# Kernel optimization log

Hardware: AMD Instinct MI355X
Metric: run time of the kernel (lower is better)

## Reference

```python
import jax, jax.numpy as jnp
import numpy as np

N, E, NG, H, BD, L, B = 4000, 50000, 12, 128, 128, 2, 100

def _gelu(x):
    return jax.nn.gelu(x, approximate=False)

def forward(pos, vel, charges, grid0, rand_SO3, batch, edge_index,
            W_basis1, b_basis1, W_basis2, b_basis2,
            W_fbasis1, b_fbasis1, W_fbasis2, b_fbasis2,
            W_embed, W_conv, W_fiber, b_conv, ln_gamma, ln_beta,
            W_ff1, b_ff1, W_ff2, b_ff2, W_ro1, b_ro1, W_ro2, b_ro2):
    n_nodes = pos.shape[0]
    n_graphs = rand_SO3.shape[0]
    n = grid0.shape[0]
    src, dst = edge_index[0], edge_index[1]
    # per-graph randomly rotated S2 grid
    grid_graph = jnp.einsum('bij,nj->bni', rand_SO3, grid0)    # [B,n,3]
    grid_node = grid_graph[batch]                               # [N,n,3]
    grid_edge = grid_node[src]                                  # [E,n,3]
    # R3S2 Euclidean invariants (separable): parallel + perpendicular parts of rel_pos wrt each grid orientation
    rel = pos[src] - pos[dst]                                   # [E,3]
    inv1 = jnp.einsum('ed,end->en', rel, grid_edge)[..., None]  # [E,n,1]
    inv2 = jnp.linalg.norm(rel[:, None, :] - inv1 * grid_edge, axis=-1, keepdims=True)
    cp = (charges[src] * charges[dst])[:, None, :]              # [E,1,1]
    ei = jnp.concatenate([inv1, inv2, jnp.broadcast_to(cp, inv1.shape)], -1)  # [E,n,3]
    # PolynomialFeatures(degree=2): [x, flatten(x outer x)] -> 3+9=12
    ei_poly = jnp.concatenate([ei, (ei[..., :, None] * ei[..., None, :]).reshape(ei.shape[:-1] + (9,))], -1)
    basis = _gelu(_gelu(ei_poly @ W_basis1 + b_basis1) @ W_basis2 + b_basis2)  # [E,n,BD]
    # fiber invariants: pairwise grid dot products (rotation cancels) -> [n,n,1]; poly deg 2 -> [n,n,2]
    fi = jnp.sum(grid0[:, None, :] * grid0[None, :, :], -1, keepdims=True)
    fi_poly = jnp.concatenate([fi, fi * fi], -1)
    fiber_basis = _gelu(_gelu(fi_poly @ W_fbasis1 + b_fbasis1) @ W_fbasis2 + b_fbasis2)  # [n,n,BD]
    # node features projected to sphere
    ones = jnp.ones((n_nodes, 1), pos.dtype)
    cnt = jax.ops.segment_sum(ones, batch, num_segments=n_graphs)
    mean_pos = jax.ops.segment_sum(pos, batch, num_segments=n_graphs) / jnp.maximum(cnt, 1.0)
    rel_pos = pos - mean_pos[batch]
    v_sph = jnp.einsum('nd,nkd->nk', vel, grid_node)[..., None]
    p_sph = jnp.einsum('nd,nkd->nk', rel_pos, grid_node)[..., None]
    c_sph = jnp.broadcast_to(charges[:, None, :], (n_nodes, n, 1))
    vn = jnp.linalg.norm(vel, axis=-1, keepdims=True)
    vn_sph = jnp.broadcast_to(vn[:, None, :], (n_nodes, n, 1))
    x = jnp.concatenate([v_sph, p_sph, c_sph, vn_sph], -1) @ W_embed  # [N,n,H]
    # SeparableBundleConvNext stack
    for l in range(W_conv.shape[0]):
        kern = basis @ W_conv[l]                                       # [E,n,H]
        x1 = jax.ops.segment_sum(x[src] * kern, dst, num_segments=n_nodes)  # depthwise spatial conv + scatter-add
        fk = fiber_basis @ W_fiber[l]                                  # [n,n,H]
        x2 = jnp.einsum('boc,poc->bpc', x1, fk) / n + b_conv[l]        # depthwise fiber conv
        mu = jnp.mean(x2, -1, keepdims=True)
        var = jnp.mean((x2 - mu) ** 2, -1, keepdims=True)
        h = (x2 - mu) / jnp.sqrt(var + 1e-5) * ln_gamma[l] + ln_beta[l]
        h = _gelu(h @ W_ff1[l] + b_ff1[l]) @ W_ff2[l] + b_ff2[l]
        x = x + h
    y = _gelu(x @ W_ro1 + b_ro1) @ W_ro2 + b_ro2                       # [N,n,1]
    return jnp.mean(grid_node * y, axis=-2)                            # sphere2vec -> [N,3]

def setup_inputs():
    key = jax.random.key(0)
    ks = jax.random.split(key, 24)
    f = jnp.float32
    # deterministic uniform-ish S2 grid (fibonacci sphere)
    i = np.arange(NG) + 0.5
    phi = np.arccos(1.0 - 2.0 * i / NG)
    th = np.pi * (1.0 + 5.0 ** 0.5) * i
    grid0 = jnp.asarray(np.stack([np.sin(phi) * np.cos(th), np.sin(phi) * np.sin(th), np.cos(phi)], -1), f)
    # random SO(3) per graph via unit quaternions
    q = jax.random.normal(ks[0], (B, 4), f)
    q = q / jnp.linalg.norm(q, axis=-1, keepdims=True)
    w, xq, yq, zq = q[:, 0], q[:, 1], q[:, 2], q[:, 3]
    R = jnp.stack([
        jnp.stack([1 - 2 * (yq ** 2 + zq ** 2), 2 * (xq * yq - zq * w), 2 * (xq * zq + yq * w)], -1),
        jnp.stack([2 * (xq * yq + zq * w), 1 - 2 * (xq ** 2 + zq ** 2), 2 * (yq * zq - xq * w)], -1),
        jnp.stack([2 * (xq * zq - yq * w), 2 * (yq * zq + xq * w), 1 - 2 * (xq ** 2 + yq ** 2)], -1)], -2)
    s = 0.05
    return dict(
        pos=jax.random.normal(ks[1], (N, 3), f),
        vel=jax.random.normal(ks[2], (N, 3), f),
        charges=jax.random.normal(ks[3], (N, 1), f),
        batch=jnp.sort(jax.random.randint(ks[4], (N,), 0, B)),
        edge_index=jax.random.randint(ks[5], (2, E), 0, N),
        grid0=grid0, rand_SO3=R,
        W_basis1=jax.random.normal(ks[6], (12, H), f) * s, b_basis1=jnp.zeros((H,), f),
        W_basis2=jax.random.normal(ks[7], (H, BD), f) * s, b_basis2=jnp.zeros((BD,), f),
        W_fbasis1=jax.random.normal(ks[8], (2, H), f) * s, b_fbasis1=jnp.zeros((H,), f),
        W_fbasis2=jax.random.normal(ks[9], (H, BD), f) * s, b_fbasis2=jnp.zeros((BD,), f),
        W_embed=jax.random.normal(ks[10], (4, H), f) * s,
        W_conv=jax.random.normal(ks[11], (L, BD, H), f) * s,
        W_fiber=jax.random.normal(ks[12], (L, BD, H), f) * s,
        b_conv=jnp.zeros((L, H), f),
        ln_gamma=jnp.ones((L, H), f), ln_beta=jnp.zeros((L, H), f),
        W_ff1=jax.random.normal(ks[13], (L, H, 4 * H), f) * s, b_ff1=jnp.zeros((L, 4 * H), f),
        W_ff2=jax.random.normal(ks[14], (L, 4 * H, H), f) * s, b_ff2=jnp.zeros((L, H), f),
        W_ro1=jax.random.normal(ks[15], (H, H), f) * s, b_ro1=jnp.zeros((H,), f),
        W_ro2=jax.random.normal(ks[16], (H, 1), f) * s, b_ro2=jnp.zeros((1,), f),
    )

def reference(pos, vel, charges, batch, edge_index, grid0, rand_SO3,
              W_basis1, b_basis1, W_basis2, b_basis2,
              W_fbasis1, b_fbasis1, W_fbasis2, b_fbasis2,
              W_embed, W_conv, W_fiber, b_conv, ln_gamma, ln_beta,
              W_ff1, b_ff1, W_ff2, b_ff2, W_ro1, b_ro1, W_ro2, b_ro2):
    return forward(pos, vel, charges, grid0, rand_SO3, batch, edge_index,
                   W_basis1, b_basis1, W_basis2, b_basis2,
                   W_fbasis1, b_fbasis1, W_fbasis2, b_fbasis2,
                   W_embed, W_conv, W_fiber, b_conv, ln_gamma, ln_beta,
                   W_ff1, b_ff1, W_ff2, b_ff2, W_ro1, b_ro1, W_ro2, b_ro2)
```

## Files before the change

kernel.cpp:

```cpp
#include <hip/hip_runtime.h>

typedef unsigned short u16;
typedef short s16x8 __attribute__((ext_vector_type(8)));
typedef float f32x4 __attribute__((ext_vector_type(4)));

constexpr int NNODES = 4000;
constexpr int NEDGES = 50000;
constexpr int NGRID  = 12;
constexpr int HD     = 128;
constexpr int H4     = 512;
constexpr int NLAY   = 2;

constexpr size_t OFF_GN   = 0;
constexpr size_t OFF_PS   = 144000;
constexpr size_t OFF_CNT  = 144304;
constexpr size_t OFF_FK   = 144512;
constexpr size_t OFF_X    = 181376;
constexpr size_t OFF_X1   = 6325376;
constexpr size_t OFF_WB   = 12469376;
constexpr size_t OFF_ROWP = 12625024;
constexpr size_t OFF_DEG  = 12629032;
constexpr size_t OFF_CUR  = 12633032;
constexpr size_t OFF_ESRT = 12637032;
constexpr size_t OFF_EIPB = 12687032;
constexpr size_t OFF_W1T  = 17487416;
constexpr size_t OFF_SRCS = 17489464;
constexpr size_t OFF_END_SLOW = 17539464;
constexpr size_t OFF_BAS  = 17539464;
constexpr size_t KERN_F   = 38400000;
constexpr size_t OFF_END_FAST  = OFF_BAS + KERN_F;
constexpr size_t OFF_END_DUAL  = OFF_BAS + 2*KERN_F;

constexpr size_t WB_W2T = 0;
constexpr size_t WB_WCT = 16384;
constexpr size_t WB_F1T = 49152;
constexpr size_t WB_F2T = 180224;

__device__ __forceinline__ u16 f2bf(float f){
  union { float f; unsigned int i; } v; v.f = f;
  unsigned int x = v.i;
  x += 0x7fffu + ((x >> 16) & 1u);
  return (u16)(x >> 16);
}
__device__ __forceinline__ float bf2f(u16 u){
  union { unsigned int i; float f; } v; v.i = ((unsigned int)u) << 16; return v.f;
}
__device__ __forceinline__ float gelu_f(float x){
  return 0.5f * x * (1.0f + erff(x * 0.70710678118654752f));
}
__device__ __forceinline__ float waveReduceSum(float v){
  #pragma unroll
  for(int off = 32; off > 0; off >>= 1) v += __shfl_xor(v, off, 64);
  return v;
}
__device__ __forceinline__ f32x4 mfma16(s16x8 a, s16x8 b, f32x4 c){
  return __builtin_amdgcn_mfma_f32_16x16x32_bf16(a, b, c, 0, 0, 0);
}

__global__ void k_stats(const float* __restrict__ pos, const int* __restrict__ batch,
                        float* __restrict__ possum, float* __restrict__ pcnt){
  int n = blockIdx.x * 256 + threadIdx.x;
  if(n >= NNODES) return;
  int b = batch[n];
  atomicAdd(&possum[b*3+0], pos[n*3+0]);
  atomicAdd(&possum[b*3+1], pos[n*3+1]);
  atomicAdd(&possum[b*3+2], pos[n*3+2]);
  atomicAdd(&pcnt[b], 1.0f);
}

__global__ void k_gridnode(const float* __restrict__ g0, const float* __restrict__ R,
                           const int* __restrict__ batch, float* __restrict__ grid_node){
  int idx = blockIdx.x * 256 + threadIdx.x;
  if(idx >= NNODES*NGRID) return;
  int n = idx / NGRID, k = idx % NGRID;
  int b = batch[n];
  float g[3];
  #pragma unroll
  for(int j=0;j<3;j++) g[j] = g0[k*3+j];
  #pragma unroll
  for(int i=0;i<3;i++){
    float s = 0.f;
    #pragma unroll
    for(int j=0;j<3;j++) s += R[b*9+i*3+j] * g[j];
    grid_node[idx*3+i] = s;
  }
}

__global__ __launch_bounds__(128) void k_embed(
    const float* __restrict__ pos, const float* __restrict__ vel, const float* __restrict__ charges,
    const int* __restrict__ batch, const float* __restrict__ possum, const float* __restrict__ pcnt,
    const float* __restrict__ grid_node, const float* __restrict__ W_embed, float* __restrict__ x)
{
  int n = blockIdx.x; int t = threadIdx.x;
  __shared__ float feats[NGRID][4];
  __shared__ float sgn[NGRID][3];
  if(t < 36) sgn[t/3][t%3] = grid_node[n*36 + t];
  __syncthreads();
  if(t < NGRID){
    int b = batch[n];
    float inv = 1.0f / fmaxf(pcnt[b], 1.0f);
    float v0=vel[n*3], v1=vel[n*3+1], v2=vel[n*3+2];
    float p0=pos[n*3]   - possum[b*3]*inv;
    float p1=pos[n*3+1] - possum[b*3+1]*inv;
    float p2=pos[n*3+2] - possum[b*3+2]*inv;
    float g0=sgn[t][0], g1=sgn[t][1], g2=sgn[t][2];
    feats[t][0] = v0*g0 + v1*g1 + v2*g2;
    feats[t][1] = p0*g0 + p1*g1 + p2*g2;
    feats[t][2] = charges[n];
    feats[t][3] = sqrtf(v0*v0 + v1*v1 + v2*v2);
  }
  __syncthreads();
  float w0=W_embed[0*HD+t], w1=W_embed[1*HD+t];
  float w2=W_embed[2*HD+t], w3=W_embed[3*HD+t];
  #pragma unroll
  for(int k=0;k<NGRID;k++)
    x[(n*NGRID+k)*HD + t] = feats[k][0]*w0 + feats[k][1]*w1 + feats[k][2]*w2 + feats[k][3]*w3;
}

__global__ __launch_bounds__(128) void k_fiber(
    const float* __restrict__ g0, const float* __restrict__ Wf1, const float* __restrict__ bfb1,
    const float* __restrict__ Wf2, const float* __restrict__ bfb2, const float* __restrict__ W_fiber,
    float* __restrict__ fk)
{
  int po = blockIdx.x; int p = po / NGRID, o = po % NGRID; int c = threadIdx.x;
  __shared__ float st[HD];
  __shared__ float sfb[HD];
  float fi = 0.f;
  #pragma unroll
  for(int j=0;j<3;j++) fi += g0[p*3+j] * g0[o*3+j];
  float f2 = fi*fi;
  st[c] = gelu_f(fi*Wf1[c] + f2*Wf1[HD+c] + bfb1[c]);
  __syncthreads();
  float a = bfb2[c];
  for(int j=0;j<HD;j++) a += st[j] * Wf2[j*HD+c];
  sfb[c] = gelu_f(a);
  __syncthreads();
  for(int l=0;l<NLAY;l++){
    float s = 0.f;
    for(int j=0;j<HD;j++) s += sfb[j] * W_fiber[l*HD*HD + j*HD + c];
    fk[(l*144 + po)*HD + c] = s;
  }
}

__global__ void k_prep(const float* __restrict__ W_b2, const float* __restrict__ W_b1,
                       const float* __restrict__ W_conv, const float* __restrict__ W_ff1,
                       const float* __restrict__ W_ff2,
                       u16* __restrict__ W2T, u16* __restrict__ W1T, u16* __restrict__ WCT,
                       u16* __restrict__ F1T, u16* __restrict__ F2T){
  int idx = blockIdx.x * 256 + threadIdx.x;
  if(idx < 16384){
    int r = idx >> 7, c = idx & 127;
    W2T[c*128 + r] = f2bf(W_b2[idx]);
    return;
  }
  idx -= 16384;
  if(idx < 4096){
    int c = idx >> 5, f = idx & 31;
    W1T[idx] = (f < 12) ? f2bf(W_b1[f*HD + c]) : (u16)0;
    return;
  }
  idx -= 4096;
  if(idx < 32768){
    int l = idx >> 14, j = idx & 16383;
    int r = j >> 7, c = j & 127;
    WCT[l*16384 + c*128 + r] = f2bf(W_conv[l*16384 + j]);
    return;
  }
  idx -= 32768;
  if(idx < 131072){
    int l = idx >> 16, j = idx & 65535;
    int r = j / 512, c = j % 512;
    F1T[l*65536 + c*128 + r] = f2bf(W_ff1[l*65536 + j]);
    return;
  }
  idx -= 131072;
  if(idx < 131072){
    int l = idx >> 16, j = idx & 65535;
    int r = j / 128, c = j % 128;
    F2T[l*65536 + c*512 + r] = f2bf(W_ff2[l*65536 + j]);
  }
}

__global__ void k_deg(const int* __restrict__ eidx, int* __restrict__ deg){
  int e = blockIdx.x * 256 + threadIdx.x;
  if(e >= NEDGES) return;
  atomicAdd(&deg[eidx[NEDGES + e]], 1);
}

__global__ __launch_bounds__(256) void k_scan(const int* __restrict__ deg, int* __restrict__ rowptr){
  int t = threadIdx.x;
  __shared__ int part[256];
  int base = t * 16;
  int lp[16]; int s = 0;
  #pragma unroll
  for(int i=0;i<16;i++){
    int idx = base + i;
    int v = (idx < NNODES) ? deg[idx] : 0;
    lp[i] = s; s += v;
  }
  part[t] = s;
  __syncthreads();
  for(int off=1; off<256; off<<=1){
    int v2 = (t >= off) ? part[t-off] : 0;
    __syncthreads();
    part[t] += v2;
    __syncthreads();
  }
  int excl = part[t] - s;
  #pragma unroll
  for(int i=0;i<16;i++){
    int idx = base + i;
    if(idx < NNODES) rowptr[idx] = excl + lp[i];
  }
  if(t == 255) rowptr[NNODES] = part[255];
}

__global__ void k_bucket(const int* __restrict__ eidx, const int* __restrict__ rowptr,
                         int* __restrict__ cur, int* __restrict__ esorted, int* __restrict__ srcs){
  int e = blockIdx.x * 256 + threadIdx.x;
  if(e >= NEDGES) return;
  int d = eidx[NEDGES + e];
  int p = atomicAdd(&cur[d], 1);
  int slot = rowptr[d] + p;
  esorted[slot] = e;
  srcs[slot] = eidx[e];
}

__global__ void k_einv(const int* __restrict__ esorted, const int* __restrict__ eidx,
                       const float* __restrict__ pos, const float* __restrict__ charges,
                       const float* __restrict__ grid_node, u16* __restrict__ eipb){
  int row = blockIdx.x * 256 + threadIdx.x;
  if(row >= NEDGES*NGRID) return;
  int p = row / NGRID, kg = row - p*NGRID;
  int e = esorted[p];
  int sr = eidx[e], ds = eidx[NEDGES + e];
  float r0 = pos[sr*3]   - pos[ds*3];
  float r1 = pos[sr*3+1] - pos[ds*3+1];
  float r2 = pos[sr*3+2] - pos[ds*3+2];
  float cp = charges[sr] * charges[ds];
  float g0 = grid_node[sr*36 + kg*3];
  float g1 = grid_node[sr*36 + kg*3 + 1];
  float g2 = grid_node[sr*36 + kg*3 + 2];
  float inv1 = r0*g0 + r1*g1 + r2*g2;
  float d0 = r0 - inv1*g0, d1 = r1 - inv1*g1, d2 = r2 - inv1*g2;
  float inv2 = sqrtf(d0*d0 + d1*d1 + d2*d2);
  float ei[3] = {inv1, inv2, cp};
  s16x8 lo, hi;
  #pragma unroll
  for(int i=0;i<3;i++) lo[i] = (short)f2bf(ei[i]);
  lo[3] = (short)f2bf(ei[0]*ei[0]);
  lo[4] = (short)f2bf(ei[0]*ei[1]);
  lo[5] = (short)f2bf(ei[0]*ei[2]);
  lo[6] = (short)f2bf(ei[1]*ei[0]);
  lo[7] = (short)f2bf(ei[1]*ei[1]);
  hi[0] = (short)f2bf(ei[1]*ei[2]);
  hi[1] = (short)f2bf(ei[2]*ei[0]);
  hi[2] = (short)f2bf(ei[2]*ei[1]);
  hi[3] = (short)f2bf(ei[2]*ei[2]);
  hi[4] = 0; hi[5] = 0; hi[6] = 0; hi[7] = 0;
  *(s16x8*)&eipb[(size_t)row*16]     = lo;
  *(s16x8*)&eipb[(size_t)row*16 + 8] = hi;
}

constexpr int T1S = 136;

__global__ __launch_bounds__(256) void k_kern(
    const u16* __restrict__ eipb, const u16* __restrict__ W1T,
    const float* __restrict__ b1, const float* __restrict__ b2,
    const u16* __restrict__ W2T, const u16* __restrict__ WCT,
    u16* __restrict__ kern, int nl, size_t kstride)
{
  int t = threadIdx.x;
  int lane = t & 63, w = t >> 6, quad = lane >> 4, l16 = lane & 15;
  size_t R0 = (size_t)blockIdx.x * 64;
  __shared__ __align__(16) u16 s_buf[64*T1S];

  float b1v[2], b2v[2];
  #pragma unroll
  for(int nt=0;nt<2;nt++){
    b1v[nt] = b1[(2*w+nt)*16 + l16];
    b2v[nt] = b2[(2*w+nt)*16 + l16];
  }
  const s16x8 zvec = {0,0,0,0,0,0,0,0};

  {
    f32x4 a1[4][2];
    #pragma unroll
    for(int mt=0;mt<4;mt++)
      #pragma unroll
      for(int nt=0;nt<2;nt++) a1[mt][nt] = (f32x4){0.f,0.f,0.f,0.f};
    s16x8 Af[4];
    #pragma unroll
    for(int mt=0;mt<4;mt++){
      s16x8 v = *(const s16x8*)&eipb[(R0 + mt*16 + l16)*16 + (quad&1)*8];
      if(quad >= 2) v = zvec;
      Af[mt] = v;
    }
    #pragma unroll
    for(int nt=0;nt<2;nt++){
      s16x8 Bf = *(const s16x8*)&W1T[((2*w+nt)*16 + l16)*32 + quad*8];
      #pragma unroll
      for(int mt=0;mt<4;mt++) a1[mt][nt] = mfma16(Af[mt], Bf, a1[mt][nt]);
    }
    #pragma unroll
    for(int mt=0;mt<4;mt++)
      #pragma unroll
      for(int nt=0;nt<2;nt++)
        #pragma unroll
        for(int i=0;i<4;i++)
          s_buf[(mt*16 + quad*4 + i)*T1S + (2*w+nt)*16 + l16] = f2bf(gelu_f(a1[mt][nt][i] + b1v[nt]));
  }
  __syncthreads();
  f32x4 a2[4][2];
  #pragma unroll
  for(int mt=0;mt<4;mt++)
    #pragma unroll
    for(int nt=0;nt<2;nt++) a2[mt][nt] = (f32x4){0.f,0.f,0.f,0.f};
  #pragma unroll
  for(int ks=0; ks<4; ks++){
    s16x8 Af[4];
    #pragma unroll
    for(int mt=0;mt<4;mt++)
      Af[mt] = *(const s16x8*)&s_buf[(mt*16 + l16)*T1S + ks*32 + quad*8];
    #pragma unroll
    for(int nt=0;nt<2;nt++){
      s16x8 Bf = *(const s16x8*)&W2T[((2*w+nt)*16 + l16)*HD + ks*32 + quad*8];
      #pragma unroll
      for(int mt=0;mt<4;mt++) a2[mt][nt] = mfma16(Af[mt], Bf, a2[mt][nt]);
    }
  }
  __syncthreads();
  #pragma unroll
  for(int mt=0;mt<4;mt++)
    #pragma unroll
    for(int nt=0;nt<2;nt++)
      #pragma unroll
      for(int i=0;i<4;i++)
        s_buf[(mt*16 + quad*4 + i)*T1S + (2*w+nt)*16 + l16] = f2bf(gelu_f(a2[mt][nt][i] + b2v[nt]));
  __syncthreads();
  for(int l=0; l<nl; l++){
    f32x4 a3[4][2];
    #pragma unroll
    for(int mt=0;mt<4;mt++)
      #pragma unroll
      for(int nt=0;nt<2;nt++) a3[mt][nt] = (f32x4){0.f,0.f,0.f,0.f};
    #pragma unroll
    for(int ks=0; ks<4; ks++){
      s16x8 Af[4];
      #pragma unroll
      for(int mt=0;mt<4;mt++)
        Af[mt] = *(const s16x8*)&s_buf[(mt*16 + l16)*T1S + ks*32 + quad*8];
      #pragma unroll
      for(int nt=0;nt<2;nt++){
        s16x8 Bf = *(const s16x8*)&WCT[l*16384 + ((2*w+nt)*16 + l16)*HD + ks*32 + quad*8];
        #pragma unroll
        for(int mt=0;mt<4;mt++) a3[mt][nt] = mfma16(Af[mt], Bf, a3[mt][nt]);
      }
    }
    #pragma unroll
    for(int mt=0;mt<4;mt++)
      #pragma unroll
      for(int nt=0;nt<2;nt++)
        #pragma unroll
        for(int i=0;i<4;i++)
          kern[l*kstride + (R0 + mt*16 + quad*4 + i)*HD + (2*w+nt)*16 + l16] = f2bf(a3[mt][nt][i]);
  }
}

__global__ __launch_bounds__(256) void k_gather(
    const u16* __restrict__ kern, const float* __restrict__ x,
    const int* __restrict__ rowptr, const int* __restrict__ srcs,
    float* __restrict__ x1o)
{
  int n = blockIdx.x, t = threadIdx.x;
  int c = t & 127, half = t >> 7;
  int base = rowptr[n];
  int d = rowptr[n+1] - base;
  float acc[6] = {0.f,0.f,0.f,0.f,0.f,0.f};
  int srcn = (d > 0) ? srcs[base] : 0;
  for(int e=0; e<d; e++){
    int nsrc = (e+1 < d) ? srcs[base+e+1] : 0;
    const u16*   kp = &kern[((size_t)(base+e)*NGRID + half*6)*HD + c];
    const float* xp = &x[((size_t)srcn*NGRID + half*6)*HD + c];
    #pragma unroll
    for(int kk=0;kk<6;kk++)
      acc[kk] += bf2f(kp[kk*HD]) * xp[kk*HD];
    srcn = nsrc;
  }
  #pragma unroll
  for(int kk=0;kk<6;kk++)
    x1o[((size_t)n*NGRID + half*6 + kk)*HD + c] = acc[kk];
}

__global__ __launch_bounds__(256) void k_conv_slow(
    const u16* __restrict__ eipb, const u16* __restrict__ W1T,
    const float* __restrict__ b1, const float* __restrict__ b2,
    const u16* __restrict__ W2T, const u16* __restrict__ WCT,
    const float* __restrict__ x,
    const int* __restrict__ rowptr, const int* __restrict__ srcs,
    float* __restrict__ x1o)
{
  int n = blockIdx.x; int t = threadIdx.x;
  int lane = t & 63, w = t >> 6, quad = lane >> 4, l16 = lane & 15;

  __shared__ __align__(16) u16 s_t1h[48*T1S];
  __shared__ __align__(16) u16 s_bas[48*T1S];
  __shared__ __align__(16) float accLDS[NGRID*HD];

  int base = rowptr[n];
  int d = rowptr[n+1] - base;

  float b1v[2], b2v[2];
  #pragma unroll
  for(int nt=0;nt<2;nt++){
    b1v[nt] = b1[(2*w+nt)*16 + l16];
    b2v[nt] = b2[(2*w+nt)*16 + l16];
  }

  for(int i=t; i<NGRID*HD; i+=256) accLDS[i] = 0.f;
  __syncthreads();

  f32x4 accv[3][2];
  #pragma unroll
  for(int mt=0;mt<3;mt++)
    #pragma unroll
    for(int nt=0;nt<2;nt++) accv[mt][nt] = (f32x4){0.f,0.f,0.f,0.f};

  const s16x8 zvec = {0,0,0,0,0,0,0,0};

  for(int ch=0; ch<d; ch+=4){
    size_t rowb = (size_t)(base + ch) * NGRID;
    s16x8 Af1[3];
    #pragma unroll
    for(int mt=0;mt<3;mt++){
      s16x8 v = *(const s16x8*)&eipb[(rowb + mt*16 + l16)*16 + (quad&1)*8];
      if(quad >= 2) v = zvec;
      Af1[mt] = v;
    }
    float xv[3][4][2];
    #pragma unroll
    for(int mt=0;mt<3;mt++)
      #pragma unroll
      for(int i=0;i<4;i++){
        int row = mt*16 + quad*4 + i;
        int e = row / 12;
        int k = row - e*12;
        int ei2 = base + ch + e;
        int srcn = srcs[min(ei2, NEDGES-1)];
        float m = (ch + e < d) ? 1.0f : 0.0f;
        const float* xp = &x[((size_t)srcn*NGRID + k)*HD + l16];
        #pragma unroll
        for(int nt=0;nt<2;nt++)
          xv[mt][i][nt] = xp[(2*w+nt)*16] * m;
      }
    {
      f32x4 a1[3][2];
      #pragma unroll
      for(int mt=0;mt<3;mt++)
        #pragma unroll
        for(int nt=0;nt<2;nt++) a1[mt][nt] = (f32x4){0.f,0.f,0.f,0.f};
      #pragma unroll
      for(int nt=0;nt<2;nt++){
        s16x8 Bf = *(const s16x8*)&W1T[((2*w+nt)*16 + l16)*32 + quad*8];
        #pragma unroll
        for(int mt=0;mt<3;mt++) a1[mt][nt] = mfma16(Af1[mt], Bf, a1[mt][nt]);
      }
      #pragma unroll
      for(int mt=0;mt<3;mt++)
        #pragma unroll
        for(int nt=0;nt<2;nt++)
          #pragma unroll
          for(int i=0;i<4;i++)
            s_t1h[(mt*16 + quad*4 + i)*T1S + (2*w+nt)*16 + l16] = f2bf(gelu_f(a1[mt][nt][i] + b1v[nt]));
    }
    __syncthreads();
    {
      f32x4 a2[3][2];
      #pragma unroll
      for(int mt=0;mt<3;mt++)
        #pragma unroll
        for(int nt=0;nt<2;nt++) a2[mt][nt] = (f32x4){0.f,0.f,0.f,0.f};
      #pragma unroll
      for(int ks=0; ks<4; ks++){
        s16x8 Af[3];
        #pragma unroll
        for(int mt=0;mt<3;mt++)
          Af[mt] = *(const s16x8*)&s_t1h[(mt*16 + l16)*T1S + ks*32 + quad*8];
        #pragma unroll
        for(int nt=0;nt<2;nt++){
          s16x8 Bf = *(const s16x8*)&W2T[((2*w+nt)*16 + l16)*HD + ks*32 + quad*8];
          #pragma unroll
          for(int mt=0;mt<3;mt++) a2[mt][nt] = mfma16(Af[mt], Bf, a2[mt][nt]);
        }
      }
      #pragma unroll
      for(int mt=0;mt<3;mt++)
        #pragma unroll
        for(int nt=0;nt<2;nt++)
          #pragma unroll
          for(int i=0;i<4;i++)
            s_bas[(mt*16 + quad*4 + i)*T1S + (2*w+nt)*16 + l16] = f2bf(gelu_f(a2[mt][nt][i] + b2v[nt]));
    }
    __syncthreads();
    {
      f32x4 a3[3][2];
      #pragma unroll
      for(int mt=0;mt<3;mt++)
        #pragma unroll
        for(int nt=0;nt<2;nt++) a3[mt][nt] = (f32x4){0.f,0.f,0.f,0.f};
      #pragma unroll
      for(int ks=0; ks<4; ks++){
        s16x8 Af[3];
        #pragma unroll
        for(int mt=0;mt<3;mt++)
          Af[mt] = *(const s16x8*)&s_bas[(mt*16 + l16)*T1S + ks*32 + quad*8];
        #pragma unroll
        for(int nt=0;nt<2;nt++){
          s16x8 Bf = *(const s16x8*)&WCT[((2*w+nt)*16 + l16)*HD + ks*32 + quad*8];
          #pragma unroll
          for(int mt=0;mt<3;mt++) a3[mt][nt] = mfma16(Af[mt], Bf, a3[mt][nt]);
        }
      }
      #pragma unroll
      for(int mt=0;mt<3;mt++)
        #pragma unroll
        for(int nt=0;nt<2;nt++)
          #pragma unroll
          for(int i=0;i<4;i++)
            accv[mt][nt][i] += a3[mt][nt][i] * xv[mt][i][nt];
    }
  }
  __syncthreads();
  #pragma unroll
  for(int mt=0;mt<3;mt++)
    #pragma unroll
    for(int nt=0;nt<2;nt++)
      #pragma unroll
      for(int i=0;i<4;i++){
        int row = mt*16 + quad*4 + i;
        int k = row % 12;
        atomicAdd(&accLDS[k*HD + (2*w+nt)*16 + l16], accv[mt][nt][i]);
      }
  __syncthreads();
  for(int i=t; i<NGRID*HD; i+=256)
    x1o[(size_t)n*NGRID*HD + i] = accLDS[i];
}

constexpr int STS = 520;
__global__ __launch_bounds__(256) void k_ffln(
    const u16* __restrict__ F1T, const float* __restrict__ bf1,
    const u16* __restrict__ F2T, const float* __restrict__ bf2,
    const float* __restrict__ x1raw,
    const float* __restrict__ fkl, const float* __restrict__ bconv,
    const float* __restrict__ gamma, const float* __restrict__ beta,
    float* __restrict__ x)
{
  int n = blockIdx.x; int t = threadIdx.x;
  int lane = t & 63, w = t >> 6, quad = lane >> 4, l16 = lane & 15;
  __shared__ __align__(16) float raw[NGRID*HD];
  __shared__ __align__(16) u16 sxh[16*T1S];
  __shared__ __align__(16) u16 st[16*STS];

  for(int i=t; i<NGRID*HD; i+=256) raw[i] = x1raw[(size_t)n*NGRID*HD + i];
  for(int i=t; i<4*T1S; i+=256) sxh[12*T1S + i] = 0;
  __syncthreads();

  {
    int c0 = lane, c1 = lane + 64;
    float bc0 = bconv[c0], bc1 = bconv[c1];
    float ga0 = gamma[c0], ga1 = gamma[c1];
    float be0 = beta[c0],  be1 = beta[c1];
    #pragma unroll
    for(int pp=0; pp<3; pp++){
      int p = w + pp*4;
      float a0 = 0.f, a1 = 0.f;
      #pragma unroll
      for(int o=0;o<NGRID;o++){
        a0 += raw[o*HD + c0] * fkl[(p*NGRID+o)*HD + c0];
        a1 += raw[o*HD + c1] * fkl[(p*NGRID+o)*HD + c1];
      }
      float v0 = a0 * (1.0f/12.0f) + bc0;
      float v1 = a1 * (1.0f/12.0f) + bc1;
      float mu = waveReduceSum(v0 + v1) * (1.0f/128.0f);
      float d0 = v0 - mu, d1 = v1 - mu;
      float var = waveReduceSum(d0*d0 + d1*d1) * (1.0f/128.0f);
      float inv = 1.0f / sqrtf(var + 1e-5f);
      sxh[p*T1S + c0] = f2bf(d0 * inv * ga0 + be0);
      sxh[p*T1S + c1] = f2bf(d1 * inv * ga1 + be1);
    }
  }
  __syncthreads();
  {
    f32x4 acc1[8];
    #pragma unroll
    for(int j=0;j<8;j++) acc1[j] = (f32x4){0.f,0.f,0.f,0.f};
    #pragma unroll
    for(int ks=0; ks<4; ks++){
      s16x8 Af = *(const s16x8*)&sxh[l16*T1S + ks*32 + quad*8];
      #pragma unroll
      for(int j=0;j<8;j++){
        int nt = w*8 + j;
        s16x8 Bf = *(const s16x8*)&F1T[((size_t)(nt*16 + l16))*HD + ks*32 + quad*8];
        acc1[j] = mfma16(Af, Bf, acc1[j]);
      }
    }
    #pragma unroll
    for(int j=0;j<8;j++){
      int col = (w*8+j)*16 + l16;
      float bv = bf1[col];
      #pragma unroll
      for(int i=0;i<4;i++){
        int row = quad*4 + i;
        st[row*STS + col] = f2bf(gelu_f(acc1[j][i] + bv));
      }
    }
  }
  __syncthreads();
  {
    f32x4 acc2[2];
    #pragma unroll
    for(int j=0;j<2;j++) acc2[j] = (f32x4){0.f,0.f,0.f,0.f};
    for(int ks=0; ks<16; ks++){
      s16x8 Af = *(const s16x8*)&st[l16*STS + ks*32 + quad*8];
      #pragma unroll
      for(int j=0;j<2;j++){
        int nt = w*2 + j;
        s16x8 Bf = *(const s16x8*)&F2T[((size_t)(nt*16 + l16))*H4 + ks*32 + quad*8];
        acc2[j] = mfma16(Af, Bf, acc2[j]);
      }
    }
    #pragma unroll
    for(int j=0;j<2;j++){
      int col = (w*2+j)*16 + l16;
      float bv = bf2[col];
      #pragma unroll
      for(int i=0;i<4;i++){
        int row = quad*4 + i;
        if(row < NGRID){
          size_t idx = ((size_t)n*NGRID + row)*HD + col;
          x[idx] += acc2[j][i] + bv;
        }
      }
    }
  }
}

__global__ __launch_bounds__(128) void k_readout(
    const float* __restrict__ x, const float* __restrict__ grid_node,
    const float* __restrict__ Wr1, const float* __restrict__ br1,
    const float* __restrict__ Wr2, const float* __restrict__ br2,
    float* __restrict__ out)
{
  int n = blockIdx.x; int c = threadIdx.x;
  __shared__ float sx[NGRID][HD];
  __shared__ float sy[NGRID];
  __shared__ float red[2];
  #pragma unroll
  for(int k=0;k<NGRID;k++) sx[k][c] = x[(n*NGRID+k)*HD + c];
  __syncthreads();
  float b1v = br1[c]; float w2 = Wr2[c]; float b2v = br2[0];
  float a[NGRID];
  #pragma unroll
  for(int k=0;k<NGRID;k++) a[k] = b1v;
  for(int j=0;j<HD;j++){
    float wv = Wr1[j*HD + c];
    #pragma unroll
    for(int k=0;k<NGRID;k++) a[k] += sx[k][j] * wv;
  }
  for(int k=0;k<NGRID;k++){
    float tc = gelu_f(a[k]) * w2;
    float s = waveReduceSum(tc);
    if((c & 63) == 0) red[c>>6] = s;
    __syncthreads();
    if(c == 0) sy[k] = red[0] + red[1] + b2v;
    __syncthreads();
  }
  if(c < 3){
    float s = 0.f;
    #pragma unroll
    for(int k=0;k<NGRID;k++) s += grid_node[(n*NGRID+k)*3 + c] * sy[k];
    out[n*3+c] = s * (1.0f/12.0f);
  }
}

extern "C" void kernel_launch(void* const* d_in, const int* in_sizes, int n_in,
                              void* d_out, int out_size, void* d_ws, size_t ws_size,
                              hipStream_t stream)
{
  const float* pos      = (const float*)d_in[0];
  const float* vel      = (const float*)d_in[1];
  const float* charges  = (const float*)d_in[2];
  const int*   batch    = (const int*)d_in[3];
  const int*   eidx     = (const int*)d_in[4];
  const float* grid0    = (const float*)d_in[5];
  const float* R        = (const float*)d_in[6];
  const float* W_b1     = (const float*)d_in[7];
  const float* b_b1     = (const float*)d_in[8];
  const float* W_b2     = (const float*)d_in[9];
  const float* b_b2     = (const float*)d_in[10];
  const float* W_fb1    = (const float*)d_in[11];
  const float* b_fb1    = (const float*)d_in[12];
  const float* W_fb2    = (const float*)d_in[13];
  const float* b_fb2    = (const float*)d_in[14];
  const float* W_embed  = (const float*)d_in[15];
  const float* W_conv   = (const float*)d_in[16];
  const float* W_fiber  = (const float*)d_in[17];
  const float* b_conv   = (const float*)d_in[18];
  const float* ln_g     = (const float*)d_in[19];
  const float* ln_b     = (const float*)d_in[20];
  const float* W_ff1    = (const float*)d_in[21];
  const float* b_ff1    = (const float*)d_in[22];
  const float* W_ff2    = (const float*)d_in[23];
  const float* b_ff2    = (const float*)d_in[24];
  const float* W_ro1    = (const float*)d_in[25];
  const float* b_ro1    = (const float*)d_in[26];
  const float* W_ro2    = (const float*)d_in[27];
  const float* b_ro2    = (const float*)d_in[28];

  float* ws        = (float*)d_ws;
  float* grid_node = ws + OFF_GN;
  float* possum    = ws + OFF_PS;
  float* pcnt      = ws + OFF_CNT;
  float* fk        = ws + OFF_FK;
  float* x         = ws + OFF_X;
  float* x1        = ws + OFF_X1;
  u16*   WB        = (u16*)(ws + OFF_WB);
  u16*   W2T       = WB + WB_W2T;
  u16*   WCT       = WB + WB_WCT;
  u16*   F1T       = WB + WB_F1T;
  u16*   F2T       = WB + WB_F2T;
  int*   rowptr    = (int*)(ws + OFF_ROWP);
  int*   deg       = (int*)(ws + OFF_DEG);
  int*   cur       = (int*)(ws + OFF_CUR);
  int*   esorted   = (int*)(ws + OFF_ESRT);
  u16*   eipb      = (u16*)(ws + OFF_EIPB);
  u16*   W1T       = (u16*)(ws + OFF_W1T);
  int*   srcs      = (int*)(ws + OFF_SRCS);
  u16*   kern1     = (u16*)(ws + OFF_BAS);
  const size_t KSTR = (size_t)600000 * HD;

  const bool fast = (ws_size >= OFF_END_FAST * sizeof(float));
  const bool dual = (ws_size >= OFF_END_DUAL * sizeof(float));

  hipMemsetAsync(possum, 0, 512*sizeof(float), stream);
  hipMemsetAsync(deg, 0, NNODES*sizeof(int), stream);
  hipMemsetAsync(cur, 0, NNODES*sizeof(int), stream);
  hipMemsetAsync(eipb + (size_t)NEDGES*NGRID*16, 0, 48*16*sizeof(u16), stream);

  k_stats<<<(NNODES+255)/256, 256, 0, stream>>>(pos, batch, possum, pcnt);
  k_gridnode<<<(NNODES*NGRID+255)/256, 256, 0, stream>>>(grid0, R, batch, grid_node);
  k_embed<<<NNODES, 128, 0, stream>>>(pos, vel, charges, batch, possum, pcnt, grid_node, W_embed, x);
  k_fiber<<<144, 128, 0, stream>>>(grid0, W_fb1, b_fb1, W_fb2, b_fb2, W_fiber, fk);

  k_prep<<<(315392+255)/256, 256, 0, stream>>>(W_b2, W_b1, W_conv, W_ff1, W_ff2,
                                               W2T, W1T, WCT, F1T, F2T);

  k_deg<<<(NEDGES+255)/256, 256, 0, stream>>>(eidx, deg);
  k_scan<<<1, 256, 0, stream>>>(deg, rowptr);
  k_bucket<<<(NEDGES+255)/256, 256, 0, stream>>>(eidx, rowptr, cur, esorted, srcs);

  k_einv<<<(NEDGES*NGRID+255)/256, 256, 0, stream>>>(esorted, eidx, pos, charges, grid_node, eipb);

  if(fast){
    if(dual)
      k_kern<<<9375, 256, 0, stream>>>(eipb, W1T, b_b1, b_b2, W2T, WCT, kern1, 2, KSTR);
    for(int l=0; l<NLAY; l++){
      if(!dual)
        k_kern<<<9375, 256, 0, stream>>>(eipb, W1T, b_b1, b_b2, W2T, WCT + (size_t)l*16384,
                                         kern1, 1, 0);
      const u16* kl = dual ? (kern1 + (size_t)l*KSTR) : kern1;
      k_gather<<<NNODES, 256, 0, stream>>>(kl, x, rowptr, srcs, x1);
      k_ffln<<<NNODES, 256, 0, stream>>>(F1T + (size_t)l*65536, b_ff1 + l*H4,
          F2T + (size_t)l*65536, b_ff2 + l*HD, x1,
          fk + (size_t)l*144*HD, b_conv + l*HD, ln_g + l*HD, ln_b + l*HD, x);
    }
  } else {
    for(int l=0; l<NLAY; l++){
      k_conv_slow<<<NNODES, 256, 0, stream>>>(eipb, W1T, b_b1, b_b2, W2T, WCT + (size_t)l*16384,
          x, rowptr, srcs, x1);
      k_ffln<<<NNODES, 256, 0, stream>>>(F1T + (size_t)l*65536, b_ff1 + l*H4,
          F2T + (size_t)l*65536, b_ff2 + l*HD, x1,
          fk + (size_t)l*144*HD, b_conv + l*HD, ln_g + l*HD, ln_b + l*HD, x);
    }
  }

  k_readout<<<NNODES, 128, 0, stream>>>(x, grid_node, W_ro1, b_ro1, W_ro2, b_ro2, (float*)d_out);
}
```

Baseline: 940.8 us.

## Fuse neighbor gather with fiber conv, layernorm and feed-forward per node pair

Replaces the separate gather and FF/LN kernels with one kernel that handles two nodes per block. Each block accumulates the edge kernel times neighbor features into shared memory, then runs the fiber mixing, layernorm and both MFMA feed-forward GEMMs without writing the intermediate to global memory. Processing two nodes per block fills 32 MFMA rows instead of 16, so each weight fragment load serves twice as much work. The gather now uses paired bf16/float2 loads, and ping-pong buffers replace the in-place update. The cost is more shared memory and registers per block and only half as many blocks.

Result: slower. 985.4 us (+4.7%).

```diff
diff --git a/kernel.cpp b/kernel.cpp
--- a/kernel.cpp
+++ b/kernel.cpp
@@ -367,29 +367,151 @@
   }
 }
 
-__global__ __launch_bounds__(256) void k_gather(
-    const u16* __restrict__ kern, const float* __restrict__ x,
+constexpr int STS = 520;
+__global__ __launch_bounds__(256) void k_convff(
+    const u16* __restrict__ kern, const float* __restrict__ xin,
     const int* __restrict__ rowptr, const int* __restrict__ srcs,
-    float* __restrict__ x1o)
+    const u16* __restrict__ F1T, const float* __restrict__ bf1,
+    const u16* __restrict__ F2T, const float* __restrict__ bf2,
+    const float* __restrict__ fkl, const float* __restrict__ bconv,
+    const float* __restrict__ gamma, const float* __restrict__ beta,
+    float* __restrict__ xout)
 {
-  int n = blockIdx.x, t = threadIdx.x;
-  int c = t & 127, half = t >> 7;
-  int base = rowptr[n];
-  int d = rowptr[n+1] - base;
-  float acc[6] = {0.f,0.f,0.f,0.f,0.f,0.f};
-  int srcn = (d > 0) ? srcs[base] : 0;
-  for(int e=0; e<d; e++){
-    int nsrc = (e+1 < d) ? srcs[base+e+1] : 0;
-    const u16*   kp = &kern[((size_t)(base+e)*NGRID + half*6)*HD + c];
-    const float* xp = &x[((size_t)srcn*NGRID + half*6)*HD + c];
-    #pragma unroll
-    for(int kk=0;kk<6;kk++)
-      acc[kk] += bf2f(kp[kk*HD]) * xp[kk*HD];
-    srcn = nsrc;
-  }
-  #pragma unroll
-  for(int kk=0;kk<6;kk++)
-    x1o[((size_t)n*NGRID + half*6 + kk)*HD + c] = acc[kk];
+  int t = threadIdx.x;
+  int n0 = blockIdx.x * 2;
+  __shared__ __align__(16) float raw[2*NGRID*HD];
+  __shared__ __align__(16) u16 sxh[32*T1S];
+  __shared__ __align__(16) u16 st[32*STS];
+
+  {
+    int nd = t >> 7;
+    int tt = t & 127;
+    int lane2 = (tt & 63) * 2;
+    int g = tt >> 6;
+    int n = n0 + nd;
+    int base = rowptr[n];
+    int d = rowptr[n+1] - base;
+    float2 acc[6];
+    #pragma unroll
+    for(int kk=0;kk<6;kk++){ acc[kk].x = 0.f; acc[kk].y = 0.f; }
+    int srcn = (d > 0) ? srcs[base] : 0;
+    for(int e=0; e<d; e++){
+      int nsrc = (e+1 < d) ? srcs[base+e+1] : 0;
+      const u16*   kp = &kern[((size_t)(base+e)*NGRID + g*6)*HD + lane2];
+      const float* xp = &xin[((size_t)srcn*NGRID + g*6)*HD + lane2];
+      #pragma unroll
+      for(int kk=0;kk<6;kk++){
+        unsigned int u = *(const unsigned int*)&kp[kk*HD];
+        float2 xv = *(const float2*)&xp[kk*HD];
+        acc[kk].x += bf2f((u16)(u & 0xffffu)) * xv.x;
+        acc[kk].y += bf2f((u16)(u >> 16))     * xv.y;
+      }
+      srcn = nsrc;
+    }
+    #pragma unroll
+    for(int kk=0;kk<6;kk++){
+      raw[nd*NGRID*HD + (g*6+kk)*HD + lane2]     = acc[kk].x;
+      raw[nd*NGRID*HD + (g*6+kk)*HD + lane2 + 1] = acc[kk].y;
+    }
+  }
+  for(int i=t; i<4*T1S; i+=256){ sxh[12*T1S + i] = 0; sxh[28*T1S + i] = 0; }
+  __syncthreads();
+
+  {
+    int lane = t & 63, w = t >> 6;
+    int nd = w >> 1, wi = w & 1;
+    int c0 = lane, c1 = lane + 64;
+    const float* rw = &raw[nd*NGRID*HD];
+    float bc0 = bconv[c0], bc1 = bconv[c1];
+    float ga0 = gamma[c0], ga1 = gamma[c1];
+    float be0 = beta[c0],  be1 = beta[c1];
+    #pragma unroll
+    for(int pp=0; pp<6; pp++){
+      int p = wi + pp*2;
+      float a0 = 0.f, a1 = 0.f;
+      #pragma unroll
+      for(int o=0;o<NGRID;o++){
+        a0 += rw[o*HD + c0] * fkl[(p*NGRID+o)*HD + c0];
+        a1 += rw[o*HD + c1] * fkl[(p*NGRID+o)*HD + c1];
+      }
+      float v0 = a0 * (1.0f/12.0f) + bc0;
+      float v1 = a1 * (1.0f/12.0f) + bc1;
+      float mu = waveReduceSum(v0 + v1) * (1.0f/128.0f);
+      float d0 = v0 - mu, d1 = v1 - mu;
+      float var = waveReduceSum(d0*d0 + d1*d1) * (1.0f/128.0f);
+      float inv = 1.0f / sqrtf(var + 1e-5f);
+      sxh[(nd*16 + p)*T1S + c0] = f2bf(d0 * inv * ga0 + be0);
+      sxh[(nd*16 + p)*T1S + c1] = f2bf(d1 * inv * ga1 + be1);
+    }
+  }
+  __syncthreads();
+  {
+    int lane = t & 63, w = t >> 6, quad = lane >> 4, l16 = lane & 15;
+    f32x4 acc1[2][8];
+    #pragma unroll
+    for(int mt=0;mt<2;mt++)
+      #pragma unroll
+      for(int j=0;j<8;j++) acc1[mt][j] = (f32x4){0.f,0.f,0.f,0.f};
+    #pragma unroll
+    for(int ks=0; ks<4; ks++){
+      s16x8 Af0 = *(const s16x8*)&sxh[l16*T1S + ks*32 + quad*8];
+      s16x8 Af1 = *(const s16x8*)&sxh[(16 + l16)*T1S + ks*32 + quad*8];
+      #pragma unroll
+      for(int j=0;j<8;j++){
+        int nt = w*8 + j;
+        s16x8 Bf = *(const s16x8*)&F1T[((size_t)(nt*16 + l16))*HD + ks*32 + quad*8];
+        acc1[0][j] = mfma16(Af0, Bf, acc1[0][j]);
+        acc1[1][j] = mfma16(Af1, Bf, acc1[1][j]);
+      }
+    }
+    #pragma unroll
+    for(int j=0;j<8;j++){
+      int col = (w*8+j)*16 + l16;
+      float bv = bf1[col];
+      #pragma unroll
+      for(int mt=0;mt<2;mt++)
+        #pragma unroll
+        for(int i=0;i<4;i++){
+          int row = mt*16 + quad*4 + i;
+          st[row*STS + col] = f2bf(gelu_f(acc1[mt][j][i] + bv));
+        }
+    }
+  }
+  __syncthreads();
+  {
+    int lane = t & 63, w = t >> 6, quad = lane >> 4, l16 = lane & 15;
+    f32x4 acc2[2][2];
+    #pragma unroll
+    for(int mt=0;mt<2;mt++)
+      #pragma unroll
+      for(int j=0;j<2;j++) acc2[mt][j] = (f32x4){0.f,0.f,0.f,0.f};
+    for(int ks=0; ks<16; ks++){
+      s16x8 Af0 = *(const s16x8*)&st[l16*STS + ks*32 + quad*8];
+      s16x8 Af1 = *(const s16x8*)&st[(16 + l16)*STS + ks*32 + quad*8];
+      #pragma unroll
+      for(int j=0;j<2;j++){
+        int nt = w*2 + j;
+        s16x8 Bf = *(const s16x8*)&F2T[((size_t)(nt*16 + l16))*H4 + ks*32 + quad*8];
+        acc2[0][j] = mfma16(Af0, Bf, acc2[0][j]);
+        acc2[1][j] = mfma16(Af1, Bf, acc2[1][j]);
+      }
+    }
+    #pragma unroll
+    for(int j=0;j<2;j++){
+      int col = (w*2+j)*16 + l16;
+      float bv = bf2[col];
+      #pragma unroll
+      for(int mt=0;mt<2;mt++)
+        #pragma unroll
+        for(int i=0;i<4;i++){
+          int row = quad*4 + i;
+          if(row < NGRID){
+            size_t idx = ((size_t)(n0+mt)*NGRID + row)*HD + col;
+            xout[idx] = xin[idx] + acc2[mt][j][i] + bv;
+          }
+        }
+    }
+  }
 }
 
 __global__ __launch_bounds__(256) void k_conv_slow(
@@ -546,7 +668,6 @@
     x1o[(size_t)n*NGRID*HD + i] = accLDS[i];
 }
 
-constexpr int STS = 520;
 __global__ __launch_bounds__(256) void k_ffln(
     const u16* __restrict__ F1T, const float* __restrict__ bf1,
     const u16* __restrict__ F2T, const float* __restrict__ bf2,
@@ -764,16 +885,19 @@
   if(fast){
     if(dual)
       k_kern<<<9375, 256, 0, stream>>>(eipb, W1T, b_b1, b_b2, W2T, WCT, kern1, 2, KSTR);
+    float* xa = x;
+    float* xb = x1;
     for(int l=0; l<NLAY; l++){
       if(!dual)
         k_kern<<<9375, 256, 0, stream>>>(eipb, W1T, b_b1, b_b2, W2T, WCT + (size_t)l*16384,
                                          kern1, 1, 0);
       const u16* kl = dual ? (kern1 + (size_t)l*KSTR) : kern1;
-      k_gather<<<NNODES, 256, 0, stream>>>(kl, x, rowptr, srcs, x1);
-      k_ffln<<<NNODES, 256, 0, stream>>>(F1T + (size_t)l*65536, b_ff1 + l*H4,
-          F2T + (size_t)l*65536, b_ff2 + l*HD, x1,
-          fk + (size_t)l*144*HD, b_conv + l*HD, ln_g + l*HD, ln_b + l*HD, x);
-    }
+      k_convff<<<NNODES/2, 256, 0, stream>>>(kl, xa, rowptr, srcs,
+          F1T + (size_t)l*65536, b_ff1 + l*H4, F2T + (size_t)l*65536, b_ff2 + l*HD,
+          fk + (size_t)l*144*HD, b_conv + l*HD, ln_g + l*HD, ln_b + l*HD, xb);
+      float* tmp = xa; xa = xb; xb = tmp;
+    }
+    k_readout<<<NNODES, 128, 0, stream>>>(xa, grid_node, W_ro1, b_ro1, W_ro2, b_ro2, (float*)d_out);
   } else {
     for(int l=0; l<NLAY; l++){
       k_conv_slow<<<NNODES, 256, 0, stream>>>(eipb, W1T, b_b1, b_b2, W2T, WCT + (size_t)l*16384,
@@ -782,7 +906,6 @@
           F2T + (size_t)l*65536, b_ff2 + l*HD, x1,
           fk + (size_t)l*144*HD, b_conv + l*HD, ln_g + l*HD, ln_b + l*HD, x);
     }
-  }
-
-  k_readout<<<NNODES, 128, 0, stream>>>(x, grid_node, W_ro1, b_ro1, W_ro2, b_ro2, (float*)d_out);
-}
+    k_readout<<<NNODES, 128, 0, stream>>>(x, grid_node, W_ro1, b_ro1, W_ro2, b_ro2, (float*)d_out);
+  }
+}
```

## Process two nodes per block in FFN and MFMA-based readout

Applied to the files above, without the earlier changes.

The FFN/LayerNorm kernel now handles two nodes per block, so each weight fragment loaded from global memory feeds two MFMAs, halving weight traffic per node. The readout MLP is rewritten to use bf16 MFMA with a pre-transposed bf16 copy of W_ro1, also two nodes per block, with an LDS atomic reduction for the second layer. This adds register and LDS pressure and lowers readout precision from fp32 to bf16.

After: 974.2 us. 3.5% more time.

```diff
diff --git a/kernel.cpp b/kernel.cpp
--- a/kernel.cpp
+++ b/kernel.cpp
@@ -179,6 +179,13 @@
     int r = j / 128, c = j % 128;
     F2T[l*65536 + c*512 + r] = f2bf(W_ff2[l*65536 + j]);
   }
+}
+
+__global__ void k_prepro(const float* __restrict__ W_ro1, u16* __restrict__ RO1T){
+  int idx = blockIdx.x * 256 + threadIdx.x;
+  if(idx >= 16384) return;
+  int r = idx >> 7, c = idx & 127;
+  RO1T[c*128 + r] = f2bf(W_ro1[idx]);
 }
 
 __global__ void k_deg(const int* __restrict__ eidx, int* __restrict__ deg){
@@ -555,29 +562,32 @@
     const float* __restrict__ gamma, const float* __restrict__ beta,
     float* __restrict__ x)
 {
-  int n = blockIdx.x; int t = threadIdx.x;
-  int lane = t & 63, w = t >> 6, quad = lane >> 4, l16 = lane & 15;
-  __shared__ __align__(16) float raw[NGRID*HD];
-  __shared__ __align__(16) u16 sxh[16*T1S];
-  __shared__ __align__(16) u16 st[16*STS];
-
-  for(int i=t; i<NGRID*HD; i+=256) raw[i] = x1raw[(size_t)n*NGRID*HD + i];
-  for(int i=t; i<4*T1S; i+=256) sxh[12*T1S + i] = 0;
+  int t = threadIdx.x;
+  int n0 = blockIdx.x * 2;
+  __shared__ __align__(16) float raw[2*NGRID*HD];
+  __shared__ __align__(16) u16 sxh[32*T1S];
+  __shared__ __align__(16) u16 st[32*STS];
+
+  for(int i=t; i<2*NGRID*HD; i+=256) raw[i] = x1raw[(size_t)n0*NGRID*HD + i];
+  for(int i=t; i<4*T1S; i+=256){ sxh[12*T1S + i] = 0; sxh[28*T1S + i] = 0; }
   __syncthreads();
 
   {
+    int lane = t & 63, w = t >> 6;
+    int nd = w >> 1, wi = w & 1;
     int c0 = lane, c1 = lane + 64;
+    const float* rw = &raw[nd*NGRID*HD];
     float bc0 = bconv[c0], bc1 = bconv[c1];
     float ga0 = gamma[c0], ga1 = gamma[c1];
     float be0 = beta[c0],  be1 = beta[c1];
     #pragma unroll
-    for(int pp=0; pp<3; pp++){
-      int p = w + pp*4;
+    for(int pp=0; pp<6; pp++){
+      int p = wi + pp*2;
       float a0 = 0.f, a1 = 0.f;
       #pragma unroll
       for(int o=0;o<NGRID;o++){
-        a0 += raw[o*HD + c0] * fkl[(p*NGRID+o)*HD + c0];
-        a1 += raw[o*HD + c1] * fkl[(p*NGRID+o)*HD + c1];
+        a0 += rw[o*HD + c0] * fkl[(p*NGRID+o)*HD + c0];
+        a1 += rw[o*HD + c1] * fkl[(p*NGRID+o)*HD + c1];
       }
       float v0 = a0 * (1.0f/12.0f) + bc0;
       float v1 = a1 * (1.0f/12.0f) + bc1;
@@ -585,23 +595,28 @@
       float d0 = v0 - mu, d1 = v1 - mu;
       float var = waveReduceSum(d0*d0 + d1*d1) * (1.0f/128.0f);
       float inv = 1.0f / sqrtf(var + 1e-5f);
-      sxh[p*T1S + c0] = f2bf(d0 * inv * ga0 + be0);
-      sxh[p*T1S + c1] = f2bf(d1 * inv * ga1 + be1);
+      sxh[(nd*16 + p)*T1S + c0] = f2bf(d0 * inv * ga0 + be0);
+      sxh[(nd*16 + p)*T1S + c1] = f2bf(d1 * inv * ga1 + be1);
     }
   }
   __syncthreads();
   {
-    f32x4 acc1[8];
-    #pragma unroll
-    for(int j=0;j<8;j++) acc1[j] = (f32x4){0.f,0.f,0.f,0.f};
+    int lane = t & 63, w = t >> 6, quad = lane >> 4, l16 = lane & 15;
+    f32x4 acc1[2][8];
+    #pragma unroll
+    for(int mt=0;mt<2;mt++)
+      #pragma unroll
+      for(int j=0;j<8;j++) acc1[mt][j] = (f32x4){0.f,0.f,0.f,0.f};
     #pragma unroll
     for(int ks=0; ks<4; ks++){
-      s16x8 Af = *(const s16x8*)&sxh[l16*T1S + ks*32 + quad*8];
+      s16x8 Af0 = *(const s16x8*)&sxh[l16*T1S + ks*32 + quad*8];
+      s16x8 Af1 = *(const s16x8*)&sxh[(16 + l16)*T1S + ks*32 + quad*8];
       #pragma unroll
       for(int j=0;j<8;j++){
         int nt = w*8 + j;
         s16x8 Bf = *(const s16x8*)&F1T[((size_t)(nt*16 + l16))*HD + ks*32 + quad*8];
-        acc1[j] = mfma16(Af, Bf, acc1[j]);
+        acc1[0][j] = mfma16(Af0, Bf, acc1[0][j]);
+        acc1[1][j] = mfma16(Af1, Bf, acc1[1][j]);
       }
     }
     #pragma unroll
@@ -609,24 +624,31 @@
       int col = (w*8+j)*16 + l16;
       float bv = bf1[col];
       #pragma unroll
-      for(int i=0;i<4;i++){
-        int row = quad*4 + i;
-        st[row*STS + col] = f2bf(gelu_f(acc1[j][i] + bv));
-      }
+      for(int mt=0;mt<2;mt++)
+        #pragma unroll
+        for(int i=0;i<4;i++){
+          int row = mt*16 + quad*4 + i;
+          st[row*STS + col] = f2bf(gelu_f(acc1[mt][j][i] + bv));
+        }
     }
   }
   __syncthreads();
   {
-    f32x4 acc2[2];
-    #pragma unroll
-    for(int j=0;j<2;j++) acc2[j] = (f32x4){0.f,0.f,0.f,0.f};
+    int lane = t & 63, w = t >> 6, quad = lane >> 4, l16 = lane & 15;
+    f32x4 acc2[2][2];
+    #pragma unroll
+    for(int mt=0;mt<2;mt++)
+      #pragma unroll
+      for(int j=0;j<2;j++) acc2[mt][j] = (f32x4){0.f,0.f,0.f,0.f};
     for(int ks=0; ks<16; ks++){
-      s16x8 Af = *(const s16x8*)&st[l16*STS + ks*32 + quad*8];
+      s16x8 Af0 = *(const s16x8*)&st[l16*STS + ks*32 + quad*8];
+      s16x8 Af1 = *(const s16x8*)&st[(16 + l16)*STS + ks*32 + quad*8];
       #pragma unroll
       for(int j=0;j<2;j++){
         int nt = w*2 + j;
         s16x8 Bf = *(const s16x8*)&F2T[((size_t)(nt*16 + l16))*H4 + ks*32 + quad*8];
-        acc2[j] = mfma16(Af, Bf, acc2[j]);
+        acc2[0][j] = mfma16(Af0, Bf, acc2[0][j]);
+        acc2[1][j] = mfma16(Af1, Bf, acc2[1][j]);
       }
     }
     #pragma unroll
@@ -634,52 +656,78 @@
       int col = (w*2+j)*16 + l16;
       float bv = bf2[col];
       #pragma unroll
-      for(int i=0;i<4;i++){
-        int row = quad*4 + i;
-        if(row < NGRID){
-          size_t idx = ((size_t)n*NGRID + row)*HD + col;
-          x[idx] += acc2[j][i] + bv;
+      for(int mt=0;mt<2;mt++)
+        #pragma unroll
+        for(int i=0;i<4;i++){
+          int row = quad*4 + i;
+          if(row < NGRID){
+            size_t idx = ((size_t)(n0+mt)*NGRID + row)*HD + col;
+            x[idx] += acc2[mt][j][i] + bv;
+          }
         }
-      }
-    }
-  }
-}
-
-__global__ __launch_bounds__(128) void k_readout(
+    }
+  }
+}
+
+__global__ __launch_bounds__(256) void k_readout(
     const float* __restrict__ x, const float* __restrict__ grid_node,
-    const float* __restrict__ Wr1, const float* __restrict__ br1,
+    const u16* __restrict__ RO1T, const float* __restrict__ br1,
     const float* __restrict__ Wr2, const float* __restrict__ br2,
     float* __restrict__ out)
 {
-  int n = blockIdx.x; int c = threadIdx.x;
-  __shared__ float sx[NGRID][HD];
-  __shared__ float sy[NGRID];
-  __shared__ float red[2];
-  #pragma unroll
-  for(int k=0;k<NGRID;k++) sx[k][c] = x[(n*NGRID+k)*HD + c];
-  __syncthreads();
-  float b1v = br1[c]; float w2 = Wr2[c]; float b2v = br2[0];
-  float a[NGRID];
-  #pragma unroll
-  for(int k=0;k<NGRID;k++) a[k] = b1v;
-  for(int j=0;j<HD;j++){
-    float wv = Wr1[j*HD + c];
-    #pragma unroll
-    for(int k=0;k<NGRID;k++) a[k] += sx[k][j] * wv;
-  }
-  for(int k=0;k<NGRID;k++){
-    float tc = gelu_f(a[k]) * w2;
-    float s = waveReduceSum(tc);
-    if((c & 63) == 0) red[c>>6] = s;
-    __syncthreads();
-    if(c == 0) sy[k] = red[0] + red[1] + b2v;
-    __syncthreads();
-  }
-  if(c < 3){
+  int t = threadIdx.x;
+  int n0 = blockIdx.x * 2;
+  int lane = t & 63, w = t >> 6, quad = lane >> 4, l16 = lane & 15;
+  __shared__ __align__(16) u16 sxh[32*T1S];
+  __shared__ float sy[32];
+  if(t < 32) sy[t] = 0.f;
+  for(int i=t; i<2*NGRID*HD; i+=256){
+    int nd = i / (NGRID*HD), rem = i - nd*NGRID*HD;
+    int r = rem >> 7, c = rem & 127;
+    sxh[(nd*16 + r)*T1S + c] = f2bf(x[(size_t)n0*NGRID*HD + i]);
+  }
+  for(int i=t; i<4*T1S; i+=256){ sxh[12*T1S + i] = 0; sxh[28*T1S + i] = 0; }
+  __syncthreads();
+  f32x4 acc[2][2];
+  #pragma unroll
+  for(int mt=0;mt<2;mt++)
+    #pragma unroll
+    for(int j=0;j<2;j++) acc[mt][j] = (f32x4){0.f,0.f,0.f,0.f};
+  #pragma unroll
+  for(int ks=0; ks<4; ks++){
+    s16x8 Af0 = *(const s16x8*)&sxh[l16*T1S + ks*32 + quad*8];
+    s16x8 Af1 = *(const s16x8*)&sxh[(16 + l16)*T1S + ks*32 + quad*8];
+    #pragma unroll
+    for(int j=0;j<2;j++){
+      int nt = w*2 + j;
+      s16x8 Bf = *(const s16x8*)&RO1T[((size_t)(nt*16 + l16))*HD + ks*32 + quad*8];
+      acc[0][j] = mfma16(Af0, Bf, acc[0][j]);
+      acc[1][j] = mfma16(Af1, Bf, acc[1][j]);
+    }
+  }
+  #pragma unroll
+  for(int j=0;j<2;j++){
+    int col = (w*2+j)*16 + l16;
+    float bv = br1[col];
+    float w2v = Wr2[col];
+    #pragma unroll
+    for(int mt=0;mt<2;mt++)
+      #pragma unroll
+      for(int i=0;i<4;i++){
+        int row = quad*4 + i;
+        if(row < NGRID)
+          atomicAdd(&sy[mt*16 + row], gelu_f(acc[mt][j][i] + bv) * w2v);
+      }
+  }
+  __syncthreads();
+  if(t < 6){
+    int nd = t / 3, d = t - nd*3;
+    float b2v = br2[0];
     float s = 0.f;
     #pragma unroll
-    for(int k=0;k<NGRID;k++) s += grid_node[(n*NGRID+k)*3 + c] * sy[k];
-    out[n*3+c] = s * (1.0f/12.0f);
+    for(int k=0;k<NGRID;k++)
+      s += grid_node[((size_t)(n0+nd)*NGRID + k)*3 + d] * (sy[nd*16 + k] + b2v);
+    out[(n0+nd)*3 + d] = s * (1.0f/12.0f);
   }
 }
 
@@ -737,6 +785,7 @@
   u16*   W1T       = (u16*)(ws + OFF_W1T);
   int*   srcs      = (int*)(ws + OFF_SRCS);
   u16*   kern1     = (u16*)(ws + OFF_BAS);
+  u16*   RO1T      = (u16*)(ws + OFF_ESRT);
   const size_t KSTR = (size_t)600000 * HD;
 
   const bool fast = (ws_size >= OFF_END_FAST * sizeof(float));
@@ -760,6 +809,7 @@
   k_bucket<<<(NEDGES+255)/256, 256, 0, stream>>>(eidx, rowptr, cur, esorted, srcs);
 
   k_einv<<<(NEDGES*NGRID+255)/256, 256, 0, stream>>>(esorted, eidx, pos, charges, grid_node, eipb);
+  k_prepro<<<64, 256, 0, stream>>>(W_ro1, RO1T);
 
   if(fast){
     if(dual)
@@ -770,7 +820,7 @@
                                          kern1, 1, 0);
       const u16* kl = dual ? (kern1 + (size_t)l*KSTR) : kern1;
       k_gather<<<NNODES, 256, 0, stream>>>(kl, x, rowptr, srcs, x1);
-      k_ffln<<<NNODES, 256, 0, stream>>>(F1T + (size_t)l*65536, b_ff1 + l*H4,
+      k_ffln<<<NNODES/2, 256, 0, stream>>>(F1T + (size_t)l*65536, b_ff1 + l*H4,
           F2T + (size_t)l*65536, b_ff2 + l*HD, x1,
           fk + (size_t)l*144*HD, b_conv + l*HD, ln_g + l*HD, ln_b + l*HD, x);
     }
@@ -778,11 +828,11 @@
     for(int l=0; l<NLAY; l++){
       k_conv_slow<<<NNODES, 256, 0, stream>>>(eipb, W1T, b_b1, b_b2, W2T, WCT + (size_t)l*16384,
           x, rowptr, srcs, x1);
-      k_ffln<<<NNODES, 256, 0, stream>>>(F1T + (size_t)l*65536, b_ff1 + l*H4,
+      k_ffln<<<NNODES/2, 256, 0, stream>>>(F1T + (size_t)l*65536, b_ff1 + l*H4,
           F2T + (size_t)l*65536, b_ff2 + l*HD, x1,
           fk + (size_t)l*144*HD, b_conv + l*HD, ln_g + l*HD, ln_b + l*HD, x);
     }
   }
 
-  k_readout<<<NNODES, 128, 0, stream>>>(x, grid_node, W_ro1, b_ro1, W_ro2, b_ro2, (float*)d_out);
-}
+  k_readout<<<NNODES/2, 256, 0, stream>>>(x, grid_node, RO1T, b_ro1, W_ro2, b_ro2, (float*)d_out);
+}
```
